# Performance work log

Hardware: AMD Instinct MI355X
Metric: run time of the kernel (lower is better)

Reference implementation:

```python
import jax, jax.numpy as jnp
import numpy as np

B, N, DIM, H, DH = 8, 1024, 512, 8, 64
INNER = H * DH
SCALE = DH ** -0.5


def setup_inputs() -> dict:
    key = jax.random.key(0)
    ks = jax.random.split(key, 9)
    s = 0.02
    return {
        "x": jax.random.normal(ks[0], (B, N, DIM), jnp.float32),
        "lidar": jax.random.normal(ks[1], (B, N, INNER), jnp.float32),
        "w_qkv": jax.random.normal(ks[2], (3 * INNER, DIM), jnp.float32) * s,
        "w_merge": jax.random.normal(ks[3], (DH, DH), jnp.float32) * s,
        "b_merge": jnp.zeros((DH,), jnp.float32),
        "w_out": jax.random.normal(ks[4], (DIM, INNER), jnp.float32) * s,
        "b_out": jnp.zeros((DIM,), jnp.float32),
        "conv_w": jax.random.normal(ks[5], (2,), jnp.float32) * 0.5,
        "conv_b": jnp.zeros((), jnp.float32),
    }


def _split_heads(t):  # [b, n, h*d] -> [b, h, n, d]
    b, n, _ = t.shape
    return t.reshape(b, n, H, DH).transpose(0, 2, 1, 3)


def reference(x, lidar, w_qkv, w_merge, b_merge, w_out, b_out, conv_w, conv_b):
    b, n, _ = x.shape
    qkv = x @ w_qkv.T  # [b, n, 3*inner]
    q, k, v = jnp.split(qkv, 3, axis=-1)
    q, k, v = _split_heads(q), _split_heads(k), _split_heads(v)
    lid = _split_heads(lidar)

    dots = jnp.einsum('bhid,bhjd->bhij', q, k) * SCALE
    lidar_sim = jnp.einsum('bhid,bhjd->bhij', lid, lid) * SCALE
    lidar_sim = jax.nn.softmax(lidar_sim, axis=-1)

    # 1x1 conv over 2 channels == learned linear blend of the two score maps
    mid = conv_w[0] * dots + conv_w[1] * lidar_sim + conv_b
    attn = jax.nn.softmax(mid, axis=-1)

    out = jnp.einsum('bhij,bhjd->bhid', attn, v)
    out = out @ w_merge.T + b_merge                  # per-head linear_merge
    out = out.transpose(0, 2, 1, 3).reshape(b, n, INNER)  # b h n d -> b n (h d)
    out = out @ w_out.T + b_out                      # to_out (dropout = identity)
    return (out, lidar)
```

## Files before the change

kernel.cpp:

```cpp
#include <hip/hip_runtime.h>
#include <hip/hip_bf16.h>

#define B_      8
#define N_      1024
#define DIM_    512
#define H_      8
#define DH_     64
#define INNER_  512
#define SCALE_  0.125f
#define LOG2E_  1.4426950408889634f

typedef __attribute__((ext_vector_type(8))) __bf16         bf16x8;
typedef __attribute__((ext_vector_type(8))) unsigned short ushort8;
typedef __attribute__((ext_vector_type(4))) float          f32x4;

union FragCast { ushort8 u; bf16x8 b; };
union FragU32  { unsigned int u[4]; bf16x8 b; };

__device__ inline bf16x8 ld_frag(const unsigned short* p) {
    FragCast f; f.u = *(const ushort8*)p; return f.b;
}

__device__ inline f32x4 mfma16(bf16x8 a, bf16x8 b, f32x4 c) {
    return __builtin_amdgcn_mfma_f32_16x16x32_bf16(a, b, c, 0, 0, 0);
}

__device__ inline float fexp2(float x) { return __builtin_amdgcn_exp2f(x); }

__device__ inline unsigned short f2bf(float x) {
    unsigned int u = __float_as_uint(x);
    unsigned int lsb = (u >> 16) & 1u;
    u += 0x7fffu + lsb;
    return (unsigned short)(u >> 16);
}

__device__ inline unsigned int pack_bf2(float hi, float lo) {
    return __builtin_amdgcn_perm(__float_as_uint(hi), __float_as_uint(lo), 0x07060302u);
}

__device__ inline void gl_lds(const unsigned short* g, unsigned short* l) {
    __builtin_amdgcn_global_load_lds(
        (const __attribute__((address_space(1))) unsigned int*)g,
        (__attribute__((address_space(3))) unsigned int*)l, 16, 0, 0);
}

__global__ __launch_bounds__(256) void k_convert(
    const float* __restrict__ x, const float* __restrict__ lidar,
    const float* __restrict__ wqkv, const float* __restrict__ wmerge,
    const float* __restrict__ wout,
    unsigned short* __restrict__ x_bf, unsigned short* __restrict__ lid_bf,
    float* __restrict__ out_lidar,
    unsigned short* __restrict__ wqkv_bf, unsigned short* __restrict__ wm_bf,
    unsigned short* __restrict__ wout_bf)
{
    const int bx = blockIdx.x, tid = threadIdx.x;
    const float* src; unsigned short* dst; bool isLid = false; long base;
    if (bx < 1024)      { src = x;      dst = x_bf;    base = (long)bx * 1024; }
    else if (bx < 2048) { src = lidar;  dst = lid_bf;  base = (long)(bx - 1024) * 1024; isLid = true; }
    else if (bx < 2240) { src = wqkv;   dst = wqkv_bf; base = (long)(bx - 2048) * 1024; }
    else if (bx < 2304) { src = wout;   dst = wout_bf; base = (long)(bx - 2240) * 1024; }
    else                { src = wmerge; dst = wm_bf;   base = 0; }
    for (int k = 0; k < 4; k++) {
        long j = base + k * 256 + tid;
        float4 v = ((const float4*)src)[j];
        ushort4 o;
        o.x = f2bf(v.x); o.y = f2bf(v.y); o.z = f2bf(v.z); o.w = f2bf(v.w);
        ((ushort4*)dst)[j] = o;
        if (isLid) ((float4*)out_lidar)[j] = v;
    }
}

__global__ __launch_bounds__(256) void k_gemm_qkv(
    const unsigned short* __restrict__ A, const unsigned short* __restrict__ Bm,
    unsigned short* __restrict__ C, int M, int Nd, int K)
{
    __shared__ unsigned short sA[128 * 64];
    __shared__ unsigned short sB[128 * 64];
    const int tid  = threadIdx.x;
    const int lane = tid & 63, wave = tid >> 6;
    const int q = lane >> 4, l15 = lane & 15, l7 = l15 & 7;
    const int xq0 = (q ^ l7) << 3, xq4 = ((q + 4) ^ l7) << 3;
    const int m0 = blockIdx.x * 128, n0 = blockIdx.y * 128;
    const int wm = (wave >> 1) * 64, wn = (wave & 1) * 64;
    f32x4 acc[4][4] = {};

    for (int k0 = 0; k0 < K; k0 += 64) {
        __syncthreads();
        for (int i = 0; i < 4; i++) {
            int c = i * 256 + tid;
            int row = c >> 3;
            int gcol = ((c & 7) ^ (row & 7)) << 3;
            gl_lds(&A[(long)(m0 + row) * K + k0 + gcol], &sA[c * 8]);
            gl_lds(&Bm[(long)(n0 + row) * K + k0 + gcol], &sB[c * 8]);
        }
        __syncthreads();
        for (int kk = 0; kk < 2; kk++) {
            const int xx = kk ? xq4 : xq0;
            bf16x8 af[4], bfr[4];
            for (int i = 0; i < 4; i++)
                af[i]  = ld_frag(&sA[(wm + i * 16 + l15) * 64 + xx]);
            for (int i = 0; i < 4; i++)
                bfr[i] = ld_frag(&sB[(wn + i * 16 + l15) * 64 + xx]);
            for (int mi = 0; mi < 4; mi++)
                for (int ni = 0; ni < 4; ni++)
                    acc[mi][ni] = mfma16(af[mi], bfr[ni], acc[mi][ni]);
        }
    }
    for (int mi = 0; mi < 4; mi++)
        for (int ni = 0; ni < 4; ni++)
            for (int r = 0; r < 4; r++) {
                int row = m0 + wm + mi * 16 + q * 4 + r;
                int col = n0 + wn + ni * 16 + l15;
                C[(long)row * Nd + col] = f2bf(acc[mi][ni][r]);
            }
}

__global__ __launch_bounds__(256) void k_gemm_out(
    const unsigned short* __restrict__ A, const unsigned short* __restrict__ Bm,
    const float* __restrict__ bias, float* __restrict__ C, int M, int Nd, int K)
{
    __shared__ unsigned short sA[128 * 64];
    __shared__ unsigned short sB[64 * 64];
    const int tid  = threadIdx.x;
    const int lane = tid & 63, wave = tid >> 6;
    const int q = lane >> 4, l15 = lane & 15, l7 = l15 & 7;
    const int xq0 = (q ^ l7) << 3, xq4 = ((q + 4) ^ l7) << 3;
    const int m0 = blockIdx.x * 128, n0 = blockIdx.y * 64;
    const int wm = (wave >> 1) * 64, wn = (wave & 1) * 32;
    f32x4 acc[4][2] = {};

    for (int k0 = 0; k0 < K; k0 += 64) {
        __syncthreads();
        for (int i = 0; i < 4; i++) {
            int c = i * 256 + tid;
            int row = c >> 3;
            int gcol = ((c & 7) ^ (row & 7)) << 3;
            gl_lds(&A[(long)(m0 + row) * K + k0 + gcol], &sA[c * 8]);
            if (i < 2)
                gl_lds(&Bm[(long)(n0 + row) * K + k0 + gcol], &sB[c * 8]);
        }
        __syncthreads();
        for (int kk = 0; kk < 2; kk++) {
            const int xx = kk ? xq4 : xq0;
            bf16x8 af[4], bfr[2];
            for (int i = 0; i < 4; i++)
                af[i]  = ld_frag(&sA[(wm + i * 16 + l15) * 64 + xx]);
            for (int i = 0; i < 2; i++)
                bfr[i] = ld_frag(&sB[(wn + i * 16 + l15) * 64 + xx]);
            for (int mi = 0; mi < 4; mi++)
                for (int ni = 0; ni < 2; ni++)
                    acc[mi][ni] = mfma16(af[mi], bfr[ni], acc[mi][ni]);
        }
    }
    for (int mi = 0; mi < 4; mi++)
        for (int ni = 0; ni < 2; ni++)
            for (int r = 0; r < 4; r++) {
                int row = m0 + wm + mi * 16 + q * 4 + r;
                int col = n0 + wn + ni * 16 + l15;
                C[(long)row * Nd + col] = acc[mi][ni][r] + bias[col];
            }
}

__global__ __launch_bounds__(256) void k_transpose_v(
    const unsigned short* __restrict__ qkv_bf, unsigned short* __restrict__ vt)
{
    __shared__ unsigned short sT[64 * 72];
    const int tid = threadIdx.x;
    const int tok0 = blockIdx.x * 64, f0 = blockIdx.y * 64;
    {
        int j = tid & 63, d0 = (tid >> 6) * 16;
        const unsigned short* src = &qkv_bf[(long)(tok0 + j) * 1536 + 1024 + f0 + d0];
        ushort8 v0 = *(const ushort8*)src;
        ushort8 v1 = *(const ushort8*)(src + 8);
        for (int e = 0; e < 8; e++) sT[(d0 + e) * 72 + j]     = v0[e];
        for (int e = 0; e < 8; e++) sT[(d0 + 8 + e) * 72 + j] = v1[e];
    }
    __syncthreads();
    for (int i = 0; i < 4; i++) {
        int g = i * 256 + tid;
        int fr = g >> 4, g4 = g & 15;
        int pp = (g4 >> 3) * 32 + (g4 & 3) * 8 + ((g4 >> 2) & 1) * 4;
        ushort4 o4 = *(const ushort4*)&sT[fr * 72 + g4 * 4];
        *(ushort4*)&vt[(long)(f0 + fr) * (B_ * N_) + tok0 + pp] = o4;
    }
}

__global__ __launch_bounds__(256) void k_flash(
    const unsigned short* __restrict__ qkv_bf, const unsigned short* __restrict__ lid_bf,
    const unsigned short* __restrict__ vt,
    const unsigned short* __restrict__ wm_bf, const float* __restrict__ b_merge,
    const float* __restrict__ conv_w, const float* __restrict__ conv_b,
    unsigned short* __restrict__ tmp_bf)
{
    __shared__ unsigned short sK[64 * 64];
    __shared__ unsigned short sLid[64 * 64];
    __shared__ unsigned short sVT[64 * 72];
    __shared__ unsigned short sO[4 * 16 * 72];
    __shared__ float sRS[4][16];

    const int tid = threadIdx.x, lane = tid & 63, wave = tid >> 6;
    const int q = lane >> 4, l15 = lane & 15, l7 = l15 & 7;
    const int xq0 = (q ^ l7) << 3, xq4 = ((q + 4) ^ l7) << 3;
    const int itile = blockIdx.x, bh = blockIdx.y;
    const int b = bh >> 3, h = bh & 7;
    const int i0w = itile * 64 + wave * 16;
    const long rowB = (long)b * N_;
    const int colh = h * DH_;
    const float k0c = conv_w[0] * SCALE_ * LOG2E_;
    const float k2c = conv_b[0] * LOG2E_;
    const float c1L = conv_w[1] * LOG2E_;
    const float sc = SCALE_ * LOG2E_;

    bf16x8 qf[2], lf[2];
    for (int ks = 0; ks < 2; ks++) {
        qf[ks] = ld_frag(&qkv_bf[(rowB + i0w + l15) * 1536 + colh + ks * 32 + q * 8]);
        lf[ks] = ld_frag(&lid_bf[(rowB + i0w + l15) * INNER_ + colh + ks * 32 + q * 8]);
    }

    float rsl = 0.f;
    for (int j0 = 0; j0 < N_; j0 += 64) {
        __syncthreads();
        for (int i = 0; i < 2; i++) {
            int c = i * 256 + tid;
            int row = c >> 3;
            int gcol = ((c & 7) ^ (row & 7)) << 3;
            gl_lds(&lid_bf[(rowB + j0 + row) * INNER_ + colh + gcol], &sLid[c * 8]);
        }
        __syncthreads();
        for (int ns = 0; ns < 4; ns++) {
            int rb = (ns * 16 + l15) * 64;
            f32x4 cv = {0.f, 0.f, 0.f, 0.f};
            cv = mfma16(ld_frag(&sLid[rb + xq0]), lf[0], cv);
            cv = mfma16(ld_frag(&sLid[rb + xq4]), lf[1], cv);
            for (int r = 0; r < 4; r++) rsl += fexp2(cv[r] * sc);
        }
    }
    rsl += __shfl_xor(rsl, 16);
    rsl += __shfl_xor(rsl, 32);
    const float k1 = c1L / rsl;

    float rs = 0.f;
    f32x4 o[4] = {};

    for (int j0 = 0; j0 < N_; j0 += 64) {
        __syncthreads();
        for (int i = 0; i < 2; i++) {
            int c = i * 256 + tid;
            int row = c >> 3;
            int gcol = ((c & 7) ^ (row & 7)) << 3;
            gl_lds(&qkv_bf[(rowB + j0 + row) * 1536 + 512 + colh + gcol], &sK[c * 8]);
            gl_lds(&lid_bf[(rowB + j0 + row) * INNER_ + colh + gcol], &sLid[c * 8]);
        }
        for (int i = 0; i < 2; i++) {
            int c = i * 256 + tid;
            int row = c >> 3, col = (c & 7) * 8;
            *(ushort8*)&sVT[row * 72 + col] =
                *(const ushort8*)&vt[(long)(colh + row) * (B_ * N_) + rowB + j0 + col];
        }
        __syncthreads();

        for (int ns2 = 0; ns2 < 2; ns2++) {
            unsigned int pu[4];
            for (int h2 = 0; h2 < 2; h2++) {
                int ns = ns2 * 2 + h2;
                int rb = (ns * 16 + l15) * 64;
                f32x4 a = {0.f, 0.f, 0.f, 0.f};
                a = mfma16(ld_frag(&sK[rb + xq0]), qf[0], a);
                a = mfma16(ld_frag(&sK[rb + xq4]), qf[1], a);
                f32x4 cv = {0.f, 0.f, 0.f, 0.f};
                cv = mfma16(ld_frag(&sLid[rb + xq0]), lf[0], cv);
                cv = mfma16(ld_frag(&sLid[rb + xq4]), lf[1], cv);
                float pv[4];
                for (int r = 0; r < 4; r++) {
                    float els = fexp2(cv[r] * sc);
                    float t = fmaf(k0c, a[r], k2c);
                    t = fmaf(k1, els, t);
                    pv[r] = fexp2(t);
                    rs += pv[r];
                }
                pu[h2 * 2 + 0] = pack_bf2(pv[1], pv[0]);
                pu[h2 * 2 + 1] = pack_bf2(pv[3], pv[2]);
            }
            FragU32 fa;
            fa.u[0] = pu[0]; fa.u[1] = pu[1]; fa.u[2] = pu[2]; fa.u[3] = pu[3];
            for (int dt = 0; dt < 4; dt++) {
                bf16x8 vb = ld_frag(&sVT[(dt * 16 + l15) * 72 + ns2 * 32 + q * 8]);
                o[dt] = mfma16(fa.b, vb, o[dt]);
            }
        }
    }

    rs += __shfl_xor(rs, 16);
    rs += __shfl_xor(rs, 32);
    if (q == 0) sRS[wave][l15] = rs;
    float invr[4];
    for (int r = 0; r < 4; r++) invr[r] = 1.f / sRS[wave][q * 4 + r];

    unsigned short* pO = &sO[wave * 16 * 72];
    for (int dt = 0; dt < 4; dt++)
        for (int r = 0; r < 4; r++)
            pO[(q * 4 + r) * 72 + dt * 16 + l15] = f2bf(o[dt][r] * invr[r]);

    f32x4 mo[4] = {};
    for (int ks = 0; ks < 2; ks++) {
        bf16x8 af = ld_frag(&pO[l15 * 72 + ks * 32 + q * 8]);
        for (int ns = 0; ns < 4; ns++) {
            bf16x8 wf = ld_frag(&wm_bf[(ns * 16 + l15) * 64 + ks * 32 + q * 8]);
            mo[ns] = mfma16(af, wf, mo[ns]);
        }
    }
    for (int ns = 0; ns < 4; ns++) {
        float bm = b_merge[ns * 16 + l15];
        for (int r = 0; r < 4; r++) {
            long row = rowB + i0w + q * 4 + r;
            tmp_bf[row * INNER_ + colh + ns * 16 + l15] = f2bf(mo[ns][r] + bm);
        }
    }
}

extern "C" void kernel_launch(void* const* d_in, const int* in_sizes, int n_in,
                              void* d_out, int out_size, void* d_ws, size_t ws_size,
                              hipStream_t stream) {
    const float* x       = (const float*)d_in[0];
    const float* lidar   = (const float*)d_in[1];
    const float* w_qkv   = (const float*)d_in[2];
    const float* w_merge = (const float*)d_in[3];
    const float* b_merge = (const float*)d_in[4];
    const float* w_out   = (const float*)d_in[5];
    const float* b_out   = (const float*)d_in[6];
    const float* conv_w  = (const float*)d_in[7];
    const float* conv_b  = (const float*)d_in[8];

    float* out0      = (float*)d_out;
    float* out_lidar = out0 + (long)B_ * N_ * INNER_;

    size_t off = 0;
    auto carve = [&](size_t bytes) {
        void* p = (char*)d_ws + off;
        off += (bytes + 255) & ~(size_t)255;
        return p;
    };
    unsigned short* qkv_bf  = (unsigned short*)carve((size_t)B_ * N_ * 3 * INNER_ * 2);
    unsigned short* lid_bf  = (unsigned short*)carve((size_t)B_ * N_ * INNER_ * 2);
    unsigned short* x_bf    = (unsigned short*)carve((size_t)B_ * N_ * DIM_ * 2);
    unsigned short* wqkv_bf = (unsigned short*)carve((size_t)3 * INNER_ * DIM_ * 2);
    unsigned short* wout_bf = (unsigned short*)carve((size_t)DIM_ * INNER_ * 2);
    unsigned short* wm_bf   = (unsigned short*)carve((size_t)DH_ * DH_ * 2);
    unsigned short* tmp_bf  = (unsigned short*)carve((size_t)B_ * N_ * INNER_ * 2);
    unsigned short* vt_bf   = (unsigned short*)carve((size_t)INNER_ * B_ * N_ * 2);

    k_convert<<<2305, 256, 0, stream>>>(x, lidar, w_qkv, w_merge, w_out,
                                        x_bf, lid_bf, out_lidar,
                                        wqkv_bf, wm_bf, wout_bf);

    k_gemm_qkv<<<dim3(64, 12), 256, 0, stream>>>(
        x_bf, wqkv_bf, qkv_bf, B_ * N_, 3 * INNER_, DIM_);

    k_transpose_v<<<dim3(128, 8), 256, 0, stream>>>(qkv_bf, vt_bf);

    k_flash<<<dim3(16, 64), 256, 0, stream>>>(
        qkv_bf, lid_bf, vt_bf, wm_bf, b_merge, conv_w, conv_b, tmp_bf);

    k_gemm_out<<<dim3(64, 8), 256, 0, stream>>>(
        tmp_bf, wout_bf, b_out, out0, B_ * N_, DIM_, INNER_);
}
```

Measured before the change: 203.2 us.

## Fuse V transpose into QKV GEMM epilogue and process two query tiles per wave

The QKV GEMM now writes the V third of its output directly into the transposed, permuted layout, so the separate transpose kernel is removed. The flash kernel has each wave handle two 16-row query sets, so every K, lidar and V fragment loaded from LDS feeds twice as many MFMAs. The grid is halved to match. V tiles are now loaded asynchronously with an XOR swizzle instead of a padded layout. This cuts a kernel launch, a global round trip and LDS/global traffic per unit of work, at the cost of more registers per thread and fewer blocks to fill the GPU.

```diff
diff --git a/kernel.cpp b/kernel.cpp
--- a/kernel.cpp
+++ b/kernel.cpp
@@ -72,7 +72,8 @@
 
 __global__ __launch_bounds__(256) void k_gemm_qkv(
     const unsigned short* __restrict__ A, const unsigned short* __restrict__ Bm,
-    unsigned short* __restrict__ C, int M, int Nd, int K)
+    unsigned short* __restrict__ C, unsigned short* __restrict__ vt,
+    int M, int Nd, int K)
 {
     __shared__ unsigned short sA[128 * 64];
     __shared__ unsigned short sB[128 * 64];
@@ -106,13 +107,27 @@
                     acc[mi][ni] = mfma16(af[mi], bfr[ni], acc[mi][ni]);
         }
     }
-    for (int mi = 0; mi < 4; mi++)
-        for (int ni = 0; ni < 4; ni++)
-            for (int r = 0; r < 4; r++) {
-                int row = m0 + wm + mi * 16 + q * 4 + r;
-                int col = n0 + wn + ni * 16 + l15;
-                C[(long)row * Nd + col] = f2bf(acc[mi][ni][r]);
-            }
+    if (n0 < 1024) {
+        for (int mi = 0; mi < 4; mi++)
+            for (int ni = 0; ni < 4; ni++)
+                for (int r = 0; r < 4; r++) {
+                    int row = m0 + wm + mi * 16 + q * 4 + r;
+                    int col = n0 + wn + ni * 16 + l15;
+                    C[(long)row * Nd + col] = f2bf(acc[mi][ni][r]);
+                }
+    } else {
+        for (int mi = 0; mi < 4; mi++) {
+            int pp0 = (mi >> 1) * 32 + q * 8 + (mi & 1) * 4;
+            long tbase = m0 + wm + pp0;
+            for (int ni = 0; ni < 4; ni++) {
+                int f = (n0 - 1024) + wn + ni * 16 + l15;
+                ushort4 o4;
+                o4.x = f2bf(acc[mi][ni][0]); o4.y = f2bf(acc[mi][ni][1]);
+                o4.z = f2bf(acc[mi][ni][2]); o4.w = f2bf(acc[mi][ni][3]);
+                *(ushort4*)&vt[(long)f * (B_ * N_) + tbase] = o4;
+            }
+        }
+    }
 }
 
 __global__ __launch_bounds__(256) void k_gemm_out(
@@ -161,30 +176,6 @@
             }
 }
 
-__global__ __launch_bounds__(256) void k_transpose_v(
-    const unsigned short* __restrict__ qkv_bf, unsigned short* __restrict__ vt)
-{
-    __shared__ unsigned short sT[64 * 72];
-    const int tid = threadIdx.x;
-    const int tok0 = blockIdx.x * 64, f0 = blockIdx.y * 64;
-    {
-        int j = tid & 63, d0 = (tid >> 6) * 16;
-        const unsigned short* src = &qkv_bf[(long)(tok0 + j) * 1536 + 1024 + f0 + d0];
-        ushort8 v0 = *(const ushort8*)src;
-        ushort8 v1 = *(const ushort8*)(src + 8);
-        for (int e = 0; e < 8; e++) sT[(d0 + e) * 72 + j]     = v0[e];
-        for (int e = 0; e < 8; e++) sT[(d0 + 8 + e) * 72 + j] = v1[e];
-    }
-    __syncthreads();
-    for (int i = 0; i < 4; i++) {
-        int g = i * 256 + tid;
-        int fr = g >> 4, g4 = g & 15;
-        int pp = (g4 >> 3) * 32 + (g4 & 3) * 8 + ((g4 >> 2) & 1) * 4;
-        ushort4 o4 = *(const ushort4*)&sT[fr * 72 + g4 * 4];
-        *(ushort4*)&vt[(long)(f0 + fr) * (B_ * N_) + tok0 + pp] = o4;
-    }
-}
-
 __global__ __launch_bounds__(256) void k_flash(
     const unsigned short* __restrict__ qkv_bf, const unsigned short* __restrict__ lid_bf,
     const unsigned short* __restrict__ vt,
@@ -194,7 +185,7 @@
 {
     __shared__ unsigned short sK[64 * 64];
     __shared__ unsigned short sLid[64 * 64];
-    __shared__ unsigned short sVT[64 * 72];
+    __shared__ unsigned short sVT[64 * 64];
     __shared__ unsigned short sO[4 * 16 * 72];
     __shared__ float sRS[4][16];
 
@@ -203,7 +194,6 @@
     const int xq0 = (q ^ l7) << 3, xq4 = ((q + 4) ^ l7) << 3;
     const int itile = blockIdx.x, bh = blockIdx.y;
     const int b = bh >> 3, h = bh & 7;
-    const int i0w = itile * 64 + wave * 16;
     const long rowB = (long)b * N_;
     const int colh = h * DH_;
     const float k0c = conv_w[0] * SCALE_ * LOG2E_;
@@ -211,13 +201,18 @@
     const float c1L = conv_w[1] * LOG2E_;
     const float sc = SCALE_ * LOG2E_;
 
-    bf16x8 qf[2], lf[2];
-    for (int ks = 0; ks < 2; ks++) {
-        qf[ks] = ld_frag(&qkv_bf[(rowB + i0w + l15) * 1536 + colh + ks * 32 + q * 8]);
-        lf[ks] = ld_frag(&lid_bf[(rowB + i0w + l15) * INNER_ + colh + ks * 32 + q * 8]);
-    }
-
-    float rsl = 0.f;
+    int i0s[2];
+    i0s[0] = itile * 128 + wave * 16;
+    i0s[1] = i0s[0] + 64;
+
+    bf16x8 qf[2][2], lfq[2][2];
+    for (int set = 0; set < 2; set++)
+        for (int ks = 0; ks < 2; ks++) {
+            qf[set][ks]  = ld_frag(&qkv_bf[(rowB + i0s[set] + l15) * 1536 + colh + ks * 32 + q * 8]);
+            lfq[set][ks] = ld_frag(&lid_bf[(rowB + i0s[set] + l15) * INNER_ + colh + ks * 32 + q * 8]);
+        }
+
+    float rsl[2] = {0.f, 0.f};
     for (int j0 = 0; j0 < N_; j0 += 64) {
         __syncthreads();
         for (int i = 0; i < 2; i++) {
@@ -229,18 +224,25 @@
         __syncthreads();
         for (int ns = 0; ns < 4; ns++) {
             int rb = (ns * 16 + l15) * 64;
-            f32x4 cv = {0.f, 0.f, 0.f, 0.f};
-            cv = mfma16(ld_frag(&sLid[rb + xq0]), lf[0], cv);
-            cv = mfma16(ld_frag(&sLid[rb + xq4]), lf[1], cv);
-            for (int r = 0; r < 4; r++) rsl += fexp2(cv[r] * sc);
-        }
-    }
-    rsl += __shfl_xor(rsl, 16);
-    rsl += __shfl_xor(rsl, 32);
-    const float k1 = c1L / rsl;
-
-    float rs = 0.f;
-    f32x4 o[4] = {};
+            bf16x8 af0 = ld_frag(&sLid[rb + xq0]);
+            bf16x8 af1 = ld_frag(&sLid[rb + xq4]);
+            for (int set = 0; set < 2; set++) {
+                f32x4 cv = {0.f, 0.f, 0.f, 0.f};
+                cv = mfma16(af0, lfq[set][0], cv);
+                cv = mfma16(af1, lfq[set][1], cv);
+                for (int r = 0; r < 4; r++) rsl[set] += fexp2(cv[r] * sc);
+            }
+        }
+    }
+    float k1[2];
+    for (int set = 0; set < 2; set++) {
+        rsl[set] += __shfl_xor(rsl[set], 16);
+        rsl[set] += __shfl_xor(rsl[set], 32);
+        k1[set] = c1L / rsl[set];
+    }
+
+    float rs[2] = {0.f, 0.f};
+    f32x4 o[2][4] = {};
 
     for (int j0 = 0; j0 < N_; j0 += 64) {
         __syncthreads();
@@ -250,70 +252,74 @@
             int gcol = ((c & 7) ^ (row & 7)) << 3;
             gl_lds(&qkv_bf[(rowB + j0 + row) * 1536 + 512 + colh + gcol], &sK[c * 8]);
             gl_lds(&lid_bf[(rowB + j0 + row) * INNER_ + colh + gcol], &sLid[c * 8]);
-        }
-        for (int i = 0; i < 2; i++) {
-            int c = i * 256 + tid;
-            int row = c >> 3, col = (c & 7) * 8;
-            *(ushort8*)&sVT[row * 72 + col] =
-                *(const ushort8*)&vt[(long)(colh + row) * (B_ * N_) + rowB + j0 + col];
+            gl_lds(&vt[(long)(colh + row) * (B_ * N_) + rowB + j0 + gcol], &sVT[c * 8]);
         }
         __syncthreads();
 
         for (int ns2 = 0; ns2 < 2; ns2++) {
-            unsigned int pu[4];
+            FragU32 fa[2];
             for (int h2 = 0; h2 < 2; h2++) {
                 int ns = ns2 * 2 + h2;
                 int rb = (ns * 16 + l15) * 64;
-                f32x4 a = {0.f, 0.f, 0.f, 0.f};
-                a = mfma16(ld_frag(&sK[rb + xq0]), qf[0], a);
-                a = mfma16(ld_frag(&sK[rb + xq4]), qf[1], a);
-                f32x4 cv = {0.f, 0.f, 0.f, 0.f};
-                cv = mfma16(ld_frag(&sLid[rb + xq0]), lf[0], cv);
-                cv = mfma16(ld_frag(&sLid[rb + xq4]), lf[1], cv);
-                float pv[4];
-                for (int r = 0; r < 4; r++) {
-                    float els = fexp2(cv[r] * sc);
-                    float t = fmaf(k0c, a[r], k2c);
-                    t = fmaf(k1, els, t);
-                    pv[r] = fexp2(t);
-                    rs += pv[r];
+                bf16x8 kf0 = ld_frag(&sK[rb + xq0]);
+                bf16x8 kf1 = ld_frag(&sK[rb + xq4]);
+                bf16x8 lf0 = ld_frag(&sLid[rb + xq0]);
+                bf16x8 lf1 = ld_frag(&sLid[rb + xq4]);
+                for (int set = 0; set < 2; set++) {
+                    f32x4 a = {0.f, 0.f, 0.f, 0.f};
+                    a = mfma16(kf0, qf[set][0], a);
+                    a = mfma16(kf1, qf[set][1], a);
+                    f32x4 cv = {0.f, 0.f, 0.f, 0.f};
+                    cv = mfma16(lf0, lfq[set][0], cv);
+                    cv = mfma16(lf1, lfq[set][1], cv);
+                    float pv[4];
+                    for (int r = 0; r < 4; r++) {
+                        float els = fexp2(cv[r] * sc);
+                        float t = fmaf(k0c, a[r], k2c);
+                        t = fmaf(k1[set], els, t);
+                        pv[r] = fexp2(t);
+                        rs[set] += pv[r];
+                    }
+                    fa[set].u[h2 * 2 + 0] = pack_bf2(pv[1], pv[0]);
+                    fa[set].u[h2 * 2 + 1] = pack_bf2(pv[3], pv[2]);
                 }
-                pu[h2 * 2 + 0] = pack_bf2(pv[1], pv[0]);
-                pu[h2 * 2 + 1] = pack_bf2(pv[3], pv[2]);
-            }
-            FragU32 fa;
-            fa.u[0] = pu[0]; fa.u[1] = pu[1]; fa.u[2] = pu[2]; fa.u[3] = pu[3];
+            }
             for (int dt = 0; dt < 4; dt++) {
-                bf16x8 vb = ld_frag(&sVT[(dt * 16 + l15) * 72 + ns2 * 32 + q * 8]);
-                o[dt] = mfma16(fa.b, vb, o[dt]);
-            }
-        }
-    }
-
-    rs += __shfl_xor(rs, 16);
-    rs += __shfl_xor(rs, 32);
-    if (q == 0) sRS[wave][l15] = rs;
-    float invr[4];
-    for (int r = 0; r < 4; r++) invr[r] = 1.f / sRS[wave][q * 4 + r];
+                int vrow = dt * 16 + l15;
+                bf16x8 vb = ld_frag(&sVT[vrow * 64 + (((ns2 * 4 + q) ^ l7) << 3)]);
+                o[0][dt] = mfma16(fa[0].b, vb, o[0][dt]);
+                o[1][dt] = mfma16(fa[1].b, vb, o[1][dt]);
+            }
+        }
+    }
 
     unsigned short* pO = &sO[wave * 16 * 72];
-    for (int dt = 0; dt < 4; dt++)
-        for (int r = 0; r < 4; r++)
-            pO[(q * 4 + r) * 72 + dt * 16 + l15] = f2bf(o[dt][r] * invr[r]);
-
-    f32x4 mo[4] = {};
-    for (int ks = 0; ks < 2; ks++) {
-        bf16x8 af = ld_frag(&pO[l15 * 72 + ks * 32 + q * 8]);
+    for (int set = 0; set < 2; set++) {
+        float rsv = rs[set];
+        rsv += __shfl_xor(rsv, 16);
+        rsv += __shfl_xor(rsv, 32);
+        if (q == 0) sRS[wave][l15] = rsv;
+        float invr[4];
+        for (int r = 0; r < 4; r++) invr[r] = 1.f / sRS[wave][q * 4 + r];
+
+        for (int dt = 0; dt < 4; dt++)
+            for (int r = 0; r < 4; r++)
+                pO[(q * 4 + r) * 72 + dt * 16 + l15] = f2bf(o[set][dt][r] * invr[r]);
+
+        f32x4 mo[4] = {};
+        for (int ks = 0; ks < 2; ks++) {
+            bf16x8 af = ld_frag(&pO[l15 * 72 + ks * 32 + q * 8]);
+            for (int ns = 0; ns < 4; ns++) {
+                bf16x8 wf = ld_frag(&wm_bf[(ns * 16 + l15) * 64 + ks * 32 + q * 8]);
+                mo[ns] = mfma16(af, wf, mo[ns]);
+            }
+        }
         for (int ns = 0; ns < 4; ns++) {
-            bf16x8 wf = ld_frag(&wm_bf[(ns * 16 + l15) * 64 + ks * 32 + q * 8]);
-            mo[ns] = mfma16(af, wf, mo[ns]);
-        }
-    }
-    for (int ns = 0; ns < 4; ns++) {
-        float bm = b_merge[ns * 16 + l15];
-        for (int r = 0; r < 4; r++) {
-            long row = rowB + i0w + q * 4 + r;
-            tmp_bf[row * INNER_ + colh + ns * 16 + l15] = f2bf(mo[ns][r] + bm);
+            float bm = b_merge[ns * 16 + l15];
+            for (int r = 0; r < 4; r++) {
+                long row = rowB + i0s[set] + q * 4 + r;
+                tmp_bf[row * INNER_ + colh + ns * 16 + l15] = f2bf(mo[ns][r] + bm);
+            }
         }
     }
 }
@@ -354,11 +360,9 @@
                                         wqkv_bf, wm_bf, wout_bf);
 
     k_gemm_qkv<<<dim3(64, 12), 256, 0, stream>>>(
-        x_bf, wqkv_bf, qkv_bf, B_ * N_, 3 * INNER_, DIM_);
-
-    k_transpose_v<<<dim3(128, 8), 256, 0, stream>>>(qkv_bf, vt_bf);
-
-    k_flash<<<dim3(16, 64), 256, 0, stream>>>(
+        x_bf, wqkv_bf, qkv_bf, vt_bf, B_ * N_, 3 * INNER_, DIM_);
+
+    k_flash<<<dim3(8, 64), 256, 0, stream>>>(
         qkv_bf, lid_bf, vt_bf, wm_bf, b_merge, conv_w, conv_b, tmp_bf);
 
     k_gemm_out<<<dim3(64, 8), 256, 0, stream>>>(
```

Measured after the change: 198.5 us. 2.3% less time.

## Fuse V transpose into QKV GEMM epilogue and async-load V tiles

Applied to the files above, without the earlier changes.

The QKV GEMM now writes the V third of its output directly in the transposed, permuted layout the attention kernel expects, removing the separate transpose kernel and its extra read and write of V. The flash kernel loads V tiles through the async global-to-LDS path with an XOR-swizzled layout instead of register copies into a padded buffer. The grid axes of the flash kernel are also swapped so consecutive blocks iterate over batch-heads first, which changes L2 locality. The transposed epilogue writes 8-byte scattered stores, which may coalesce poorly.

```diff
diff --git a/kernel.cpp b/kernel.cpp
--- a/kernel.cpp
+++ b/kernel.cpp
@@ -72,7 +72,8 @@
 
 __global__ __launch_bounds__(256) void k_gemm_qkv(
     const unsigned short* __restrict__ A, const unsigned short* __restrict__ Bm,
-    unsigned short* __restrict__ C, int M, int Nd, int K)
+    unsigned short* __restrict__ C, unsigned short* __restrict__ vt,
+    int M, int Nd, int K)
 {
     __shared__ unsigned short sA[128 * 64];
     __shared__ unsigned short sB[128 * 64];
@@ -106,13 +107,27 @@
                     acc[mi][ni] = mfma16(af[mi], bfr[ni], acc[mi][ni]);
         }
     }
-    for (int mi = 0; mi < 4; mi++)
-        for (int ni = 0; ni < 4; ni++)
-            for (int r = 0; r < 4; r++) {
-                int row = m0 + wm + mi * 16 + q * 4 + r;
-                int col = n0 + wn + ni * 16 + l15;
-                C[(long)row * Nd + col] = f2bf(acc[mi][ni][r]);
+    if (n0 < 1024) {
+        for (int mi = 0; mi < 4; mi++)
+            for (int ni = 0; ni < 4; ni++)
+                for (int r = 0; r < 4; r++) {
+                    int row = m0 + wm + mi * 16 + q * 4 + r;
+                    int col = n0 + wn + ni * 16 + l15;
+                    C[(long)row * Nd + col] = f2bf(acc[mi][ni][r]);
+                }
+    } else {
+        for (int mi = 0; mi < 4; mi++) {
+            int pp0 = (mi >> 1) * 32 + q * 8 + (mi & 1) * 4;
+            long tbase = m0 + wm + pp0;
+            for (int ni = 0; ni < 4; ni++) {
+                int f = (n0 - 1024) + wn + ni * 16 + l15;
+                ushort4 o4;
+                o4.x = f2bf(acc[mi][ni][0]); o4.y = f2bf(acc[mi][ni][1]);
+                o4.z = f2bf(acc[mi][ni][2]); o4.w = f2bf(acc[mi][ni][3]);
+                *(ushort4*)&vt[(long)f * (B_ * N_) + tbase] = o4;
             }
+        }
+    }
 }
 
 __global__ __launch_bounds__(256) void k_gemm_out(
@@ -161,30 +176,6 @@
             }
 }
 
-__global__ __launch_bounds__(256) void k_transpose_v(
-    const unsigned short* __restrict__ qkv_bf, unsigned short* __restrict__ vt)
-{
-    __shared__ unsigned short sT[64 * 72];
-    const int tid = threadIdx.x;
-    const int tok0 = blockIdx.x * 64, f0 = blockIdx.y * 64;
-    {
-        int j = tid & 63, d0 = (tid >> 6) * 16;
-        const unsigned short* src = &qkv_bf[(long)(tok0 + j) * 1536 + 1024 + f0 + d0];
-        ushort8 v0 = *(const ushort8*)src;
-        ushort8 v1 = *(const ushort8*)(src + 8);
-        for (int e = 0; e < 8; e++) sT[(d0 + e) * 72 + j]     = v0[e];
-        for (int e = 0; e < 8; e++) sT[(d0 + 8 + e) * 72 + j] = v1[e];
-    }
-    __syncthreads();
-    for (int i = 0; i < 4; i++) {
-        int g = i * 256 + tid;
-        int fr = g >> 4, g4 = g & 15;
-        int pp = (g4 >> 3) * 32 + (g4 & 3) * 8 + ((g4 >> 2) & 1) * 4;
-        ushort4 o4 = *(const ushort4*)&sT[fr * 72 + g4 * 4];
-        *(ushort4*)&vt[(long)(f0 + fr) * (B_ * N_) + tok0 + pp] = o4;
-    }
-}
-
 __global__ __launch_bounds__(256) void k_flash(
     const unsigned short* __restrict__ qkv_bf, const unsigned short* __restrict__ lid_bf,
     const unsigned short* __restrict__ vt,
@@ -194,14 +185,14 @@
 {
     __shared__ unsigned short sK[64 * 64];
     __shared__ unsigned short sLid[64 * 64];
-    __shared__ unsigned short sVT[64 * 72];
+    __shared__ unsigned short sVT[64 * 64];
     __shared__ unsigned short sO[4 * 16 * 72];
     __shared__ float sRS[4][16];
 
     const int tid = threadIdx.x, lane = tid & 63, wave = tid >> 6;
     const int q = lane >> 4, l15 = lane & 15, l7 = l15 & 7;
     const int xq0 = (q ^ l7) << 3, xq4 = ((q + 4) ^ l7) << 3;
-    const int itile = blockIdx.x, bh = blockIdx.y;
+    const int bh = blockIdx.x, itile = blockIdx.y;
     const int b = bh >> 3, h = bh & 7;
     const int i0w = itile * 64 + wave * 16;
     const long rowB = (long)b * N_;
@@ -211,10 +202,10 @@
     const float c1L = conv_w[1] * LOG2E_;
     const float sc = SCALE_ * LOG2E_;
 
-    bf16x8 qf[2], lf[2];
+    bf16x8 qf[2], lfq[2];
     for (int ks = 0; ks < 2; ks++) {
-        qf[ks] = ld_frag(&qkv_bf[(rowB + i0w + l15) * 1536 + colh + ks * 32 + q * 8]);
-        lf[ks] = ld_frag(&lid_bf[(rowB + i0w + l15) * INNER_ + colh + ks * 32 + q * 8]);
+        qf[ks]  = ld_frag(&qkv_bf[(rowB + i0w + l15) * 1536 + colh + ks * 32 + q * 8]);
+        lfq[ks] = ld_frag(&lid_bf[(rowB + i0w + l15) * INNER_ + colh + ks * 32 + q * 8]);
     }
 
     float rsl = 0.f;
@@ -230,8 +221,8 @@
         for (int ns = 0; ns < 4; ns++) {
             int rb = (ns * 16 + l15) * 64;
             f32x4 cv = {0.f, 0.f, 0.f, 0.f};
-            cv = mfma16(ld_frag(&sLid[rb + xq0]), lf[0], cv);
-            cv = mfma16(ld_frag(&sLid[rb + xq4]), lf[1], cv);
+            cv = mfma16(ld_frag(&sLid[rb + xq0]), lfq[0], cv);
+            cv = mfma16(ld_frag(&sLid[rb + xq4]), lfq[1], cv);
             for (int r = 0; r < 4; r++) rsl += fexp2(cv[r] * sc);
         }
     }
@@ -250,17 +241,12 @@
             int gcol = ((c & 7) ^ (row & 7)) << 3;
             gl_lds(&qkv_bf[(rowB + j0 + row) * 1536 + 512 + colh + gcol], &sK[c * 8]);
             gl_lds(&lid_bf[(rowB + j0 + row) * INNER_ + colh + gcol], &sLid[c * 8]);
-        }
-        for (int i = 0; i < 2; i++) {
-            int c = i * 256 + tid;
-            int row = c >> 3, col = (c & 7) * 8;
-            *(ushort8*)&sVT[row * 72 + col] =
-                *(const ushort8*)&vt[(long)(colh + row) * (B_ * N_) + rowB + j0 + col];
+            gl_lds(&vt[(long)(colh + row) * (B_ * N_) + rowB + j0 + gcol], &sVT[c * 8]);
         }
         __syncthreads();
 
         for (int ns2 = 0; ns2 < 2; ns2++) {
-            unsigned int pu[4];
+            FragU32 fa;
             for (int h2 = 0; h2 < 2; h2++) {
                 int ns = ns2 * 2 + h2;
                 int rb = (ns * 16 + l15) * 64;
@@ -268,8 +254,8 @@
                 a = mfma16(ld_frag(&sK[rb + xq0]), qf[0], a);
                 a = mfma16(ld_frag(&sK[rb + xq4]), qf[1], a);
                 f32x4 cv = {0.f, 0.f, 0.f, 0.f};
-                cv = mfma16(ld_frag(&sLid[rb + xq0]), lf[0], cv);
-                cv = mfma16(ld_frag(&sLid[rb + xq4]), lf[1], cv);
+                cv = mfma16(ld_frag(&sLid[rb + xq0]), lfq[0], cv);
+                cv = mfma16(ld_frag(&sLid[rb + xq4]), lfq[1], cv);
                 float pv[4];
                 for (int r = 0; r < 4; r++) {
                     float els = fexp2(cv[r] * sc);
@@ -278,13 +264,12 @@
                     pv[r] = fexp2(t);
                     rs += pv[r];
                 }
-                pu[h2 * 2 + 0] = pack_bf2(pv[1], pv[0]);
-                pu[h2 * 2 + 1] = pack_bf2(pv[3], pv[2]);
+                fa.u[h2 * 2 + 0] = pack_bf2(pv[1], pv[0]);
+                fa.u[h2 * 2 + 1] = pack_bf2(pv[3], pv[2]);
             }
-            FragU32 fa;
-            fa.u[0] = pu[0]; fa.u[1] = pu[1]; fa.u[2] = pu[2]; fa.u[3] = pu[3];
             for (int dt = 0; dt < 4; dt++) {
-                bf16x8 vb = ld_frag(&sVT[(dt * 16 + l15) * 72 + ns2 * 32 + q * 8]);
+                int vrow = dt * 16 + l15;
+                bf16x8 vb = ld_frag(&sVT[vrow * 64 + (((ns2 * 4 + q) ^ l7) << 3)]);
                 o[dt] = mfma16(fa.b, vb, o[dt]);
             }
         }
@@ -354,11 +339,9 @@
                                         wqkv_bf, wm_bf, wout_bf);
 
     k_gemm_qkv<<<dim3(64, 12), 256, 0, stream>>>(
-        x_bf, wqkv_bf, qkv_bf, B_ * N_, 3 * INNER_, DIM_);
-
-    k_transpose_v<<<dim3(128, 8), 256, 0, stream>>>(qkv_bf, vt_bf);
-
-    k_flash<<<dim3(16, 64), 256, 0, stream>>>(
+        x_bf, wqkv_bf, qkv_bf, vt_bf, B_ * N_, 3 * INNER_, DIM_);
+
+    k_flash<<<dim3(64, 16), 256, 0, stream>>>(
         qkv_bf, lid_bf, vt_bf, wm_bf, b_merge, conv_w, conv_b, tmp_bf);
 
     k_gemm_out<<<dim3(64, 8), 256, 0, stream>>>(
```

Result: faster. 198.6 us (-2.3%).
